# Performance work log

Hardware: AMD Instinct MI355X
Metric: run time of the kernel (lower is better)

## Reference

```python
import jax, jax.numpy as jnp
import numpy as np

PROB = 0.9
BRI, CON, SAT, CUT = 0.2, 0.2, 0.2, 0.25
B, C, H, W = 128, 3, 256, 256
CH = max(1, int(H * CUT))  # cutout box height = 64
CW = max(1, int(W * CUT))  # cutout box width  = 64


def setup_inputs() -> dict:
    key = jax.random.key(0)
    k = jax.random.split(key, 8)
    return {
        "images": jax.random.uniform(k[0], (B, C, H, W), jnp.float32),
        "apply_u": jax.random.uniform(k[1], (B,), jnp.float32),
        "flip_u": jax.random.uniform(k[2], (B,), jnp.float32),
        "brightness_u": jax.random.uniform(k[3], (B,), jnp.float32),
        "contrast_u": jax.random.uniform(k[4], (B,), jnp.float32),
        "saturation_u": jax.random.uniform(k[5], (B,), jnp.float32),
        "top_idx": jax.random.randint(k[6], (B,), 0, H - CH + 1, jnp.int32),
        "left_idx": jax.random.randint(k[7], (B,), 0, W - CW + 1, jnp.int32),
    }


def reference(images, apply_u, flip_u, brightness_u, contrast_u, saturation_u, top_idx, left_idx):
    x = images
    # per-sample horizontal flip (p=0.5)
    flip_mask = (flip_u < 0.5)[:, None, None, None]
    x = jnp.where(flip_mask, x[..., ::-1], x)
    # brightness: scale by uniform(1-BRI, 1+BRI)
    b = (1.0 - BRI + 2.0 * BRI * brightness_u)[:, None, None, None]
    x = x * b
    # contrast: blend with per-(sample,channel) spatial mean
    c = (1.0 - CON + 2.0 * CON * contrast_u)[:, None, None, None]
    mean = x.mean(axis=(2, 3), keepdims=True)
    x = (x - mean) * c + mean
    # saturation: blend with per-sample grayscale (channel mean), C==3
    s = (1.0 - SAT + 2.0 * SAT * saturation_u)[:, None, None, None]
    gray = x.mean(axis=1, keepdims=True)
    x = (x - gray) * s + gray
    # cutout: zero a CHxCW box at per-sample (top, left)
    rows = jnp.arange(H)[None, :, None]  # [1,H,1]
    cols = jnp.arange(W)[None, None, :]  # [1,1,W]
    t = top_idx[:, None, None]
    l = left_idx[:, None, None]
    inside = (rows >= t) & (rows < t + CH) & (cols >= l) & (cols < l + CW)  # [B,H,W]
    x = jnp.where(inside[:, None, :, :], jnp.zeros((), x.dtype), x)
    # apply augmentation only where apply_u < prob
    apply_mask = (apply_u < PROB)[:, None, None, None]
    return jnp.where(apply_mask, x, images)
```

## Files before the change

### kernel.cpp

```cpp
#include <hip/hip_runtime.h>
#include <stdint.h>

#define B_   128
#define C_   3
#define H_   256
#define W_   256
#define CH_  64
#define CW_  64
#define HW_  (H_ * W_)
#define NPLANES (B_ * C_)
#define PROB_ 0.9f

__device__ __forceinline__ float bf_lo(uint32_t u) {
    union { uint32_t u; float f; } c; c.u = u << 16; return c.f;
}
__device__ __forceinline__ float bf_hi(uint32_t u) {
    union { uint32_t u; float f; } c; c.u = u & 0xFFFF0000u; return c.f;
}
__device__ __forceinline__ float bf_val(uint16_t v) {
    union { uint32_t u; float f; } c; c.u = ((uint32_t)v) << 16; return c.f;
}
__device__ __forceinline__ uint16_t f2bf(float f) {
    union { float f; uint32_t u; } c; c.f = f;
    uint32_t u = c.u;
    return (uint16_t)((u + 0x7FFFu + ((u >> 16) & 1u)) >> 16);
}
__device__ __forceinline__ void unpack8(uint4 v, float e[8]) {
    e[0] = bf_lo(v.x); e[1] = bf_hi(v.x);
    e[2] = bf_lo(v.y); e[3] = bf_hi(v.y);
    e[4] = bf_lo(v.z); e[5] = bf_hi(v.z);
    e[6] = bf_lo(v.w); e[7] = bf_hi(v.w);
}

__device__ __forceinline__ float scal(const void* p, int b, int is_bf16) {
    if (is_bf16) return bf_val(((const uint16_t*)p)[b]);
    return ((const float*)p)[b];
}

__device__ __forceinline__ bool sniff_bf16_01(const uint16_t* u, int lane) {
    bool ok = true;
    #pragma unroll
    for (int k = 0; k < 2; ++k) {
        float v = bf_val(u[lane + 64 * k]);
        ok = ok && (v >= 0.0f) && (v < 1.0f);
    }
    unsigned long long m = __ballot(ok);
    return m == ~0ull;
}

__global__ __launch_bounds__(256) void plane_partial_kernel(
    const void* __restrict__ img, const void* __restrict__ apply_u,
    float* __restrict__ partials, int* __restrict__ flags)
{
    __shared__ int s_imgbf;
    if (threadIdx.x < 64) {
        const bool ib = sniff_bf16_01((const uint16_t*)img, threadIdx.x);
        bool sb = false;
        if (blockIdx.x == 0) sb = sniff_bf16_01((const uint16_t*)apply_u, threadIdx.x);
        if (threadIdx.x == 0) {
            s_imgbf = ib ? 1 : 0;
            if (blockIdx.x == 0) { flags[0] = ib ? 1 : 0; flags[1] = sb ? 1 : 0; }
        }
    }
    __syncthreads();
    const int imgbf = s_imgbf;
    const int plane = blockIdx.x >> 2;
    const int q     = blockIdx.x & 3;

    float s = 0.0f;
    if (imgbf) {
        const uint4* p = (const uint4*)((const uint16_t*)img + (size_t)plane * HW_)
                         + (size_t)q * 2048;
        #pragma unroll 8
        for (int i = threadIdx.x; i < 2048; i += 256) {
            float e[8]; unpack8(p[i], e);
            s += ((e[0] + e[1]) + (e[2] + e[3])) + ((e[4] + e[5]) + (e[6] + e[7]));
        }
    } else {
        const float4* p = (const float4*)((const float*)img + (size_t)plane * HW_)
                          + (size_t)q * 4096;
        #pragma unroll 8
        for (int i = threadIdx.x; i < 4096; i += 256) {
            float4 v = p[i];
            s += (v.x + v.y) + (v.z + v.w);
        }
    }

    #pragma unroll
    for (int off = 32; off > 0; off >>= 1) s += __shfl_down(s, off, 64);

    __shared__ float wsum[4];
    const int wave = threadIdx.x >> 6;
    if ((threadIdx.x & 63) == 0) wsum[wave] = s;
    __syncthreads();
    if (threadIdx.x == 0)
        partials[blockIdx.x] = (wsum[0] + wsum[1]) + (wsum[2] + wsum[3]);
}

__global__ __launch_bounds__(256) void augment_kernel(
    const void* __restrict__ img,
    const void* __restrict__ apply_u,
    const void* __restrict__ flip_u,
    const void* __restrict__ bri_u,
    const void* __restrict__ con_u,
    const void* __restrict__ sat_u,
    const int*  __restrict__ top_idx,
    const int*  __restrict__ left_idx,
    const float* __restrict__ partials,
    const int*  __restrict__ flags,
    void*       __restrict__ out)
{
    const int imgbf = __builtin_amdgcn_readfirstlane(flags[0]);
    const int scbf  = __builtin_amdgcn_readfirstlane(flags[1]);

    const int b   = blockIdx.x >> 5;
    const int rem = ((blockIdx.x & 31) << 8) + threadIdx.x;
    const int h   = rem >> 5;
    const int w0  = (rem & 31) << 3;

    const size_t base = (size_t)b * (C_ * HW_) + (size_t)h * W_ + (size_t)w0;

    const bool apply = scal(apply_u, b, scbf) < PROB_;
    if (!apply) {
        if (imgbf) {
            const uint16_t* ip = (const uint16_t*)img;
            uint16_t*       op = (uint16_t*)out;
            #pragma unroll
            for (int c = 0; c < 3; ++c)
                *(uint4*)(op + base + (size_t)c * HW_) =
                    *(const uint4*)(ip + base + (size_t)c * HW_);
        } else {
            const float* ip = (const float*)img;
            float*       op = (float*)out;
            #pragma unroll
            for (int c = 0; c < 3; ++c) {
                *(float4*)(op + base + (size_t)c * HW_)     = *(const float4*)(ip + base + (size_t)c * HW_);
                *(float4*)(op + base + (size_t)c * HW_ + 4) = *(const float4*)(ip + base + (size_t)c * HW_ + 4);
            }
        }
        return;
    }

    const bool  flip = scal(flip_u, b, scbf) < 0.5f;
    const float fb   = 0.8f + 0.4f * scal(bri_u, b, scbf);
    const float fc   = 0.8f + 0.4f * scal(con_u, b, scbf);
    const float fs   = 0.8f + 0.4f * scal(sat_u, b, scbf);
    const int   t    = top_idx[b];
    const int   l    = left_idx[b];

    const float* pp = partials + (size_t)b * 12;
    float mraw[3];
    #pragma unroll
    for (int c = 0; c < 3; ++c)
        mraw[c] = ((pp[c * 4 + 0] + pp[c * 4 + 1]) + (pp[c * 4 + 2] + pp[c * 4 + 3]))
                  * (1.0f / (float)HW_);

    const int sw = flip ? (W_ - 8 - w0) : w0;
    const size_t sbase = (size_t)b * (C_ * HW_) + (size_t)h * W_ + (size_t)sw;

    float x[3][8];
    #pragma unroll
    for (int c = 0; c < 3; ++c) {
        float e[8];
        if (imgbf) {
            uint4 v = *(const uint4*)((const uint16_t*)img + sbase + (size_t)c * HW_);
            unpack8(v, e);
        } else {
            const float* ip = (const float*)img + sbase + (size_t)c * HW_;
            float4 v0 = *(const float4*)(ip);
            float4 v1 = *(const float4*)(ip + 4);
            e[0] = v0.x; e[1] = v0.y; e[2] = v0.z; e[3] = v0.w;
            e[4] = v1.x; e[5] = v1.y; e[6] = v1.z; e[7] = v1.w;
        }
        const float m = fb * mraw[c];
        #pragma unroll
        for (int j = 0; j < 8; ++j) {
            const float src = flip ? e[7 - j] : e[j];
            x[c][j] = (src * fb - m) * fc + m;
        }
    }

    const bool row_in = (h >= t) && (h < t + CH_);
    #pragma unroll
    for (int j = 0; j < 8; ++j) {
        const float gray = (x[0][j] + x[1][j] + x[2][j]) * (1.0f / 3.0f);
        const int   w    = w0 + j;
        const bool inside = row_in && (w >= l) && (w < l + CW_);
        #pragma unroll
        for (int c = 0; c < 3; ++c) {
            const float y = (x[c][j] - gray) * fs + gray;
            x[c][j] = inside ? 0.0f : y;
        }
    }

    if (imgbf) {
        uint16_t* op = (uint16_t*)out;
        #pragma unroll
        for (int c = 0; c < 3; ++c) {
            uint4 ov;
            ov.x = (uint32_t)f2bf(x[c][0]) | ((uint32_t)f2bf(x[c][1]) << 16);
            ov.y = (uint32_t)f2bf(x[c][2]) | ((uint32_t)f2bf(x[c][3]) << 16);
            ov.z = (uint32_t)f2bf(x[c][4]) | ((uint32_t)f2bf(x[c][5]) << 16);
            ov.w = (uint32_t)f2bf(x[c][6]) | ((uint32_t)f2bf(x[c][7]) << 16);
            *(uint4*)(op + base + (size_t)c * HW_) = ov;
        }
    } else {
        float* op = (float*)out;
        #pragma unroll
        for (int c = 0; c < 3; ++c) {
            float4 v0, v1;
            v0.x = x[c][0]; v0.y = x[c][1]; v0.z = x[c][2]; v0.w = x[c][3];
            v1.x = x[c][4]; v1.y = x[c][5]; v1.z = x[c][6]; v1.w = x[c][7];
            *(float4*)(op + base + (size_t)c * HW_)     = v0;
            *(float4*)(op + base + (size_t)c * HW_ + 4) = v1;
        }
    }
}

extern "C" void kernel_launch(void* const* d_in, const int* in_sizes, int n_in,
                              void* d_out, int out_size, void* d_ws, size_t ws_size,
                              hipStream_t stream) {
    const void* img     = d_in[0];
    const void* apply_u = d_in[1];
    const void* flip_u  = d_in[2];
    const void* bri_u   = d_in[3];
    const void* con_u   = d_in[4];
    const void* sat_u   = d_in[5];
    const int*  top_i   = (const int*)d_in[6];
    const int*  left_i  = (const int*)d_in[7];
    float*      partials = (float*)d_ws;
    int*        flags    = (int*)((char*)d_ws + NPLANES * 4 * sizeof(float));

    plane_partial_kernel<<<NPLANES * 4, 256, 0, stream>>>(img, apply_u, partials, flags);

    const int total_vecs = B_ * HW_ / 8;
    augment_kernel<<<total_vecs / 256, 256, 0, stream>>>(
        img, apply_u, flip_u, bri_u, con_u, sat_u, top_i, left_i, partials, flags, d_out);
}
```

Before: 207.7 us.

## Fuse plane-mean reduction and augment into one kernel with grid barrier

Replaces the two-kernel pipeline (partial sums, then augment) with a single persistent-style kernel of 512 blocks. Each block loads its quarter-plane for all three channels, keeps the bf16 data in registers, publishes partial sums, and waits at a spin-wait global barrier on an atomic counter before applying the augmentation from the cached values. The intent is to read the image once instead of twice and drop one launch. The cost is heavy register use, a barrier that needs all 512 blocks resident at once, and a timeout fallback that recomputes full-plane sums. The fp32 path still reloads from global memory, and a memset is added to reset the counter.

Measured after the change: 242.7 us. 1.17x slower.

```diff
diff --git a/kernel.cpp b/kernel.cpp
--- a/kernel.cpp
+++ b/kernel.cpp
@@ -8,8 +8,8 @@
 #define CH_  64
 #define CW_  64
 #define HW_  (H_ * W_)
-#define NPLANES (B_ * C_)
 #define PROB_ 0.9f
+#define NBLK_ 512
 
 __device__ __forceinline__ float bf_lo(uint32_t u) {
     union { uint32_t u; float f; } c; c.u = u << 16; return c.f;
@@ -48,56 +48,7 @@
     return m == ~0ull;
 }
 
-__global__ __launch_bounds__(256) void plane_partial_kernel(
-    const void* __restrict__ img, const void* __restrict__ apply_u,
-    float* __restrict__ partials, int* __restrict__ flags)
-{
-    __shared__ int s_imgbf;
-    if (threadIdx.x < 64) {
-        const bool ib = sniff_bf16_01((const uint16_t*)img, threadIdx.x);
-        bool sb = false;
-        if (blockIdx.x == 0) sb = sniff_bf16_01((const uint16_t*)apply_u, threadIdx.x);
-        if (threadIdx.x == 0) {
-            s_imgbf = ib ? 1 : 0;
-            if (blockIdx.x == 0) { flags[0] = ib ? 1 : 0; flags[1] = sb ? 1 : 0; }
-        }
-    }
-    __syncthreads();
-    const int imgbf = s_imgbf;
-    const int plane = blockIdx.x >> 2;
-    const int q     = blockIdx.x & 3;
-
-    float s = 0.0f;
-    if (imgbf) {
-        const uint4* p = (const uint4*)((const uint16_t*)img + (size_t)plane * HW_)
-                         + (size_t)q * 2048;
-        #pragma unroll 8
-        for (int i = threadIdx.x; i < 2048; i += 256) {
-            float e[8]; unpack8(p[i], e);
-            s += ((e[0] + e[1]) + (e[2] + e[3])) + ((e[4] + e[5]) + (e[6] + e[7]));
-        }
-    } else {
-        const float4* p = (const float4*)((const float*)img + (size_t)plane * HW_)
-                          + (size_t)q * 4096;
-        #pragma unroll 8
-        for (int i = threadIdx.x; i < 4096; i += 256) {
-            float4 v = p[i];
-            s += (v.x + v.y) + (v.z + v.w);
-        }
-    }
-
-    #pragma unroll
-    for (int off = 32; off > 0; off >>= 1) s += __shfl_down(s, off, 64);
-
-    __shared__ float wsum[4];
-    const int wave = threadIdx.x >> 6;
-    if ((threadIdx.x & 63) == 0) wsum[wave] = s;
-    __syncthreads();
-    if (threadIdx.x == 0)
-        partials[blockIdx.x] = (wsum[0] + wsum[1]) + (wsum[2] + wsum[3]);
-}
-
-__global__ __launch_bounds__(256) void augment_kernel(
+__global__ __launch_bounds__(256, 2) void fused_aug_kernel(
     const void* __restrict__ img,
     const void* __restrict__ apply_u,
     const void* __restrict__ flip_u,
@@ -106,113 +57,210 @@
     const void* __restrict__ sat_u,
     const int*  __restrict__ top_idx,
     const int*  __restrict__ left_idx,
-    const float* __restrict__ partials,
-    const int*  __restrict__ flags,
+    float*      __restrict__ partials,
+    uint32_t*   __restrict__ counter,
     void*       __restrict__ out)
 {
-    const int imgbf = __builtin_amdgcn_readfirstlane(flags[0]);
-    const int scbf  = __builtin_amdgcn_readfirstlane(flags[1]);
-
-    const int b   = blockIdx.x >> 5;
-    const int rem = ((blockIdx.x & 31) << 8) + threadIdx.x;
-    const int h   = rem >> 5;
-    const int w0  = (rem & 31) << 3;
-
-    const size_t base = (size_t)b * (C_ * HW_) + (size_t)h * W_ + (size_t)w0;
+    __shared__ int   s_flags;
+    __shared__ float wsum[4][3];
+    __shared__ float s_p[12];
+    __shared__ int   s_ok;
+
+    if (threadIdx.x < 64) {
+        const bool ib = sniff_bf16_01((const uint16_t*)img, threadIdx.x);
+        const bool sb = sniff_bf16_01((const uint16_t*)apply_u, threadIdx.x);
+        if (threadIdx.x == 0) s_flags = (ib ? 1 : 0) | (sb ? 2 : 0);
+    }
+    __syncthreads();
+    const int imgbf = s_flags & 1;
+    const int scbf  = (s_flags >> 1) & 1;
+
+    const int b   = blockIdx.x >> 2;
+    const int q   = blockIdx.x & 3;
+    const int tid = threadIdx.x;
 
     const bool apply = scal(apply_u, b, scbf) < PROB_;
+    const bool flip  = apply && (scal(flip_u, b, scbf) < 0.5f);
+
+    uint4 cache[3][8];
+    float csum[3] = {0.0f, 0.0f, 0.0f};
+
+    #pragma unroll
+    for (int c = 0; c < 3; ++c) {
+        #pragma unroll
+        for (int k = 0; k < 8; ++k) {
+            const int i  = tid + 256 * k;
+            const int h  = q * 64 + (i >> 5);
+            const int w0 = (i & 31) << 3;
+            const int sw = flip ? (W_ - 8 - w0) : w0;
+            const size_t off = (size_t)(b * 3 + c) * HW_ + (size_t)h * W_ + sw;
+            if (imgbf) {
+                const uint4 v = *(const uint4*)((const uint16_t*)img + off);
+                cache[c][k] = v;
+                float e[8]; unpack8(v, e);
+                csum[c] += ((e[0] + e[1]) + (e[2] + e[3])) + ((e[4] + e[5]) + (e[6] + e[7]));
+            } else {
+                const float* ip = (const float*)img + off;
+                const float4 v0 = *(const float4*)(ip);
+                const float4 v1 = *(const float4*)(ip + 4);
+                csum[c] += ((v0.x + v0.y) + (v0.z + v0.w)) + ((v1.x + v1.y) + (v1.z + v1.w));
+            }
+        }
+    }
+
+    #pragma unroll
+    for (int c = 0; c < 3; ++c) {
+        float s = csum[c];
+        #pragma unroll
+        for (int off = 32; off > 0; off >>= 1) s += __shfl_down(s, off, 64);
+        if ((tid & 63) == 0) wsum[tid >> 6][c] = s;
+    }
+    __syncthreads();
+    if (tid < 3) {
+        const float v = (wsum[0][tid] + wsum[1][tid]) + (wsum[2][tid] + wsum[3][tid]);
+        __hip_atomic_store(&partials[blockIdx.x * 3 + tid], v,
+                           __ATOMIC_RELEASE, __HIP_MEMORY_SCOPE_AGENT);
+    }
+    __syncthreads();
+
+    if (tid == 0) {
+        __hip_atomic_fetch_add(counter, 1u, __ATOMIC_ACQ_REL, __HIP_MEMORY_SCOPE_AGENT);
+        int ok = 0;
+        for (int it = 0; it < 20000; ++it) {
+            if (__hip_atomic_load(counter, __ATOMIC_ACQUIRE, __HIP_MEMORY_SCOPE_AGENT)
+                >= (uint32_t)NBLK_) { ok = 1; break; }
+            __builtin_amdgcn_s_sleep(2);
+        }
+        s_ok = ok;
+    }
+    __syncthreads();
+
+    float mraw[3];
+    if (s_ok) {
+        if (tid < 12)
+            s_p[tid] = __hip_atomic_load(&partials[b * 12 + tid],
+                                         __ATOMIC_ACQUIRE, __HIP_MEMORY_SCOPE_AGENT);
+        __syncthreads();
+        #pragma unroll
+        for (int c = 0; c < 3; ++c)
+            mraw[c] = ((s_p[0 + c] + s_p[3 + c]) + (s_p[6 + c] + s_p[9 + c]))
+                      * (1.0f / (float)HW_);
+    } else {
+        #pragma unroll
+        for (int c = 0; c < 3; ++c) {
+            float s = 0.0f;
+            if (imgbf) {
+                const uint4* p = (const uint4*)((const uint16_t*)img + (size_t)(b * 3 + c) * HW_);
+                for (int i = tid; i < HW_ / 8; i += 256) {
+                    float e[8]; unpack8(p[i], e);
+                    s += ((e[0] + e[1]) + (e[2] + e[3])) + ((e[4] + e[5]) + (e[6] + e[7]));
+                }
+            } else {
+                const float4* p = (const float4*)((const float*)img + (size_t)(b * 3 + c) * HW_);
+                for (int i = tid; i < HW_ / 4; i += 256) {
+                    float4 v = p[i];
+                    s += (v.x + v.y) + (v.z + v.w);
+                }
+            }
+            #pragma unroll
+            for (int off = 32; off > 0; off >>= 1) s += __shfl_down(s, off, 64);
+            if ((tid & 63) == 0) wsum[tid >> 6][c] = s;
+        }
+        __syncthreads();
+        #pragma unroll
+        for (int c = 0; c < 3; ++c)
+            mraw[c] = ((wsum[0][c] + wsum[1][c]) + (wsum[2][c] + wsum[3][c]))
+                      * (1.0f / (float)HW_);
+    }
+
     if (!apply) {
-        if (imgbf) {
-            const uint16_t* ip = (const uint16_t*)img;
-            uint16_t*       op = (uint16_t*)out;
-            #pragma unroll
-            for (int c = 0; c < 3; ++c)
-                *(uint4*)(op + base + (size_t)c * HW_) =
-                    *(const uint4*)(ip + base + (size_t)c * HW_);
-        } else {
-            const float* ip = (const float*)img;
-            float*       op = (float*)out;
+        #pragma unroll
+        for (int c = 0; c < 3; ++c) {
+            #pragma unroll
+            for (int k = 0; k < 8; ++k) {
+                const int i  = tid + 256 * k;
+                const int h  = q * 64 + (i >> 5);
+                const int w0 = (i & 31) << 3;
+                const size_t off = (size_t)(b * 3 + c) * HW_ + (size_t)h * W_ + w0;
+                if (imgbf) {
+                    *(uint4*)((uint16_t*)out + off) = cache[c][k];
+                } else {
+                    const float* ip = (const float*)img + off;
+                    float*       op = (float*)out + off;
+                    *(float4*)(op)     = *(const float4*)(ip);
+                    *(float4*)(op + 4) = *(const float4*)(ip + 4);
+                }
+            }
+        }
+        return;
+    }
+
+    const float fb = 0.8f + 0.4f * scal(bri_u, b, scbf);
+    const float fc = 0.8f + 0.4f * scal(con_u, b, scbf);
+    const float fs = 0.8f + 0.4f * scal(sat_u, b, scbf);
+    const int   tt = top_idx[b];
+    const int   ll = left_idx[b];
+
+    #pragma unroll
+    for (int k = 0; k < 8; ++k) {
+        const int i  = tid + 256 * k;
+        const int h  = q * 64 + (i >> 5);
+        const int w0 = (i & 31) << 3;
+        const bool row_in = (h >= tt) && (h < tt + CH_);
+
+        float x[3][8];
+        #pragma unroll
+        for (int c = 0; c < 3; ++c) {
+            float e[8];
+            if (imgbf) {
+                unpack8(cache[c][k], e);
+            } else {
+                const int sw = flip ? (W_ - 8 - w0) : w0;
+                const float* ip = (const float*)img
+                                  + (size_t)(b * 3 + c) * HW_ + (size_t)h * W_ + sw;
+                const float4 v0 = *(const float4*)(ip);
+                const float4 v1 = *(const float4*)(ip + 4);
+                e[0] = v0.x; e[1] = v0.y; e[2] = v0.z; e[3] = v0.w;
+                e[4] = v1.x; e[5] = v1.y; e[6] = v1.z; e[7] = v1.w;
+            }
+            const float m = fb * mraw[c];
+            #pragma unroll
+            for (int j = 0; j < 8; ++j) {
+                const float src = flip ? e[7 - j] : e[j];
+                x[c][j] = (src * fb - m) * fc + m;
+            }
+        }
+
+        #pragma unroll
+        for (int j = 0; j < 8; ++j) {
+            const float gray = (x[0][j] + x[1][j] + x[2][j]) * (1.0f / 3.0f);
+            const int   w    = w0 + j;
+            const bool inside = row_in && (w >= ll) && (w < ll + CW_);
             #pragma unroll
             for (int c = 0; c < 3; ++c) {
-                *(float4*)(op + base + (size_t)c * HW_)     = *(const float4*)(ip + base + (size_t)c * HW_);
-                *(float4*)(op + base + (size_t)c * HW_ + 4) = *(const float4*)(ip + base + (size_t)c * HW_ + 4);
-            }
-        }
-        return;
-    }
-
-    const bool  flip = scal(flip_u, b, scbf) < 0.5f;
-    const float fb   = 0.8f + 0.4f * scal(bri_u, b, scbf);
-    const float fc   = 0.8f + 0.4f * scal(con_u, b, scbf);
-    const float fs   = 0.8f + 0.4f * scal(sat_u, b, scbf);
-    const int   t    = top_idx[b];
-    const int   l    = left_idx[b];
-
-    const float* pp = partials + (size_t)b * 12;
-    float mraw[3];
-    #pragma unroll
-    for (int c = 0; c < 3; ++c)
-        mraw[c] = ((pp[c * 4 + 0] + pp[c * 4 + 1]) + (pp[c * 4 + 2] + pp[c * 4 + 3]))
-                  * (1.0f / (float)HW_);
-
-    const int sw = flip ? (W_ - 8 - w0) : w0;
-    const size_t sbase = (size_t)b * (C_ * HW_) + (size_t)h * W_ + (size_t)sw;
-
-    float x[3][8];
-    #pragma unroll
-    for (int c = 0; c < 3; ++c) {
-        float e[8];
-        if (imgbf) {
-            uint4 v = *(const uint4*)((const uint16_t*)img + sbase + (size_t)c * HW_);
-            unpack8(v, e);
-        } else {
-            const float* ip = (const float*)img + sbase + (size_t)c * HW_;
-            float4 v0 = *(const float4*)(ip);
-            float4 v1 = *(const float4*)(ip + 4);
-            e[0] = v0.x; e[1] = v0.y; e[2] = v0.z; e[3] = v0.w;
-            e[4] = v1.x; e[5] = v1.y; e[6] = v1.z; e[7] = v1.w;
-        }
-        const float m = fb * mraw[c];
-        #pragma unroll
-        for (int j = 0; j < 8; ++j) {
-            const float src = flip ? e[7 - j] : e[j];
-            x[c][j] = (src * fb - m) * fc + m;
-        }
-    }
-
-    const bool row_in = (h >= t) && (h < t + CH_);
-    #pragma unroll
-    for (int j = 0; j < 8; ++j) {
-        const float gray = (x[0][j] + x[1][j] + x[2][j]) * (1.0f / 3.0f);
-        const int   w    = w0 + j;
-        const bool inside = row_in && (w >= l) && (w < l + CW_);
-        #pragma unroll
-        for (int c = 0; c < 3; ++c) {
-            const float y = (x[c][j] - gray) * fs + gray;
-            x[c][j] = inside ? 0.0f : y;
-        }
-    }
-
-    if (imgbf) {
-        uint16_t* op = (uint16_t*)out;
-        #pragma unroll
-        for (int c = 0; c < 3; ++c) {
-            uint4 ov;
-            ov.x = (uint32_t)f2bf(x[c][0]) | ((uint32_t)f2bf(x[c][1]) << 16);
-            ov.y = (uint32_t)f2bf(x[c][2]) | ((uint32_t)f2bf(x[c][3]) << 16);
-            ov.z = (uint32_t)f2bf(x[c][4]) | ((uint32_t)f2bf(x[c][5]) << 16);
-            ov.w = (uint32_t)f2bf(x[c][6]) | ((uint32_t)f2bf(x[c][7]) << 16);
-            *(uint4*)(op + base + (size_t)c * HW_) = ov;
-        }
-    } else {
-        float* op = (float*)out;
-        #pragma unroll
-        for (int c = 0; c < 3; ++c) {
-            float4 v0, v1;
-            v0.x = x[c][0]; v0.y = x[c][1]; v0.z = x[c][2]; v0.w = x[c][3];
-            v1.x = x[c][4]; v1.y = x[c][5]; v1.z = x[c][6]; v1.w = x[c][7];
-            *(float4*)(op + base + (size_t)c * HW_)     = v0;
-            *(float4*)(op + base + (size_t)c * HW_ + 4) = v1;
+                const float y = (x[c][j] - gray) * fs + gray;
+                x[c][j] = inside ? 0.0f : y;
+            }
+        }
+
+        #pragma unroll
+        for (int c = 0; c < 3; ++c) {
+            const size_t off = (size_t)(b * 3 + c) * HW_ + (size_t)h * W_ + w0;
+            if (imgbf) {
+                uint4 ov;
+                ov.x = (uint32_t)f2bf(x[c][0]) | ((uint32_t)f2bf(x[c][1]) << 16);
+                ov.y = (uint32_t)f2bf(x[c][2]) | ((uint32_t)f2bf(x[c][3]) << 16);
+                ov.z = (uint32_t)f2bf(x[c][4]) | ((uint32_t)f2bf(x[c][5]) << 16);
+                ov.w = (uint32_t)f2bf(x[c][6]) | ((uint32_t)f2bf(x[c][7]) << 16);
+                *(uint4*)((uint16_t*)out + off) = ov;
+            } else {
+                float4 v0, v1;
+                v0.x = x[c][0]; v0.y = x[c][1]; v0.z = x[c][2]; v0.w = x[c][3];
+                v1.x = x[c][4]; v1.y = x[c][5]; v1.z = x[c][6]; v1.w = x[c][7];
+                float* op = (float*)out + off;
+                *(float4*)(op)     = v0;
+                *(float4*)(op + 4) = v1;
+            }
         }
     }
 }
@@ -229,11 +277,11 @@
     const int*  top_i   = (const int*)d_in[6];
     const int*  left_i  = (const int*)d_in[7];
     float*      partials = (float*)d_ws;
-    int*        flags    = (int*)((char*)d_ws + NPLANES * 4 * sizeof(float));
-
-    plane_partial_kernel<<<NPLANES * 4, 256, 0, stream>>>(img, apply_u, partials, flags);
-
-    const int total_vecs = B_ * HW_ / 8;
-    augment_kernel<<<total_vecs / 256, 256, 0, stream>>>(
-        img, apply_u, flip_u, bri_u, con_u, sat_u, top_i, left_i, partials, flags, d_out);
-}
+    uint32_t*   counter  = (uint32_t*)((char*)d_ws + 8192);
+
+    hipMemsetAsync(counter, 0, sizeof(uint32_t), stream);
+
+    fused_aug_kernel<<<NBLK_, 256, 0, stream>>>(
+        img, apply_u, flip_u, bri_u, con_u, sat_u, top_i, left_i,
+        partials, counter, d_out);
+}
```
